# Kernel tuning notes

Measured on AMD Instinct MI355X. Metric: run time of the kernel, lower is better.

The kernel has to match this reference:

```python
import jax, jax.numpy as jnp
import numpy as np

N, E, F, D, H, L = 10000, 160000, 64, 32, 128, 2
DEG_HIST = np.zeros(17, np.float32); DEG_HIST[16] = N  # all nodes degree 16
BINS = np.arange(17, dtype=np.float32)
AVG_DEG_LOG = float((np.log(BINS + 1.0) * DEG_HIST).sum() / DEG_HIST.sum())
EPS_BN = 1e-5
EPS_STD = 1e-5


def setup_inputs() -> dict:
    key = jax.random.key(0)
    ks = iter(jax.random.split(key, 16))
    def w(shape, s=0.05):
        return jax.random.normal(next(ks), shape, dtype=jnp.float32) * s
    return {
        'x': jax.random.normal(next(ks), (N, F), dtype=jnp.float32),
        'edge_index': jax.random.randint(next(ks), (2, E), 0, N, dtype=jnp.int32),
        'edge_attr': jax.random.normal(next(ks), (E, D), dtype=jnp.float32),
        'W_node': w((F, H)), 'b_node': jnp.zeros((H,), jnp.float32),
        'W_edge': w((D, H)), 'b_edge': jnp.zeros((H,), jnp.float32),
        'W_ee': w((L, H, H)), 'b_ee': jnp.zeros((L, H), jnp.float32),
        'W_pre': w((L, 3 * H, H)), 'b_pre': jnp.zeros((L, H), jnp.float32),
        'W_post': w((L, 13 * H, H)), 'b_post': jnp.zeros((L, H), jnp.float32),
        'W_lin': w((L, H, H)), 'b_lin': jnp.zeros((L, H), jnp.float32),
        'gamma': jnp.ones((L, H), jnp.float32), 'beta': jnp.zeros((L, H), jnp.float32),
        'We1': w((L, 3 * H, H)), 'be1': jnp.zeros((L, H), jnp.float32),
        'We2': w((L, H, H)), 'be2': jnp.zeros((L, H), jnp.float32),
    }


def _pna_layer(x, edge_attr, src, dst, p):
    (W_ee, b_ee, W_pre, b_pre, W_post, b_post, W_lin, b_lin,
     gamma, beta, We1, be1, We2, be2) = p
    # message: pre-MLP on [x_i (dst), x_j (src), encoded edge_attr]
    e_enc = edge_attr @ W_ee + b_ee                                   # [E,H]
    h = jnp.concatenate([x[dst], x[src], e_enc], axis=-1) @ W_pre + b_pre  # [E,H]
    # multi-aggregator scatter at dst
    cnt = jax.ops.segment_sum(jnp.ones((E,), h.dtype), dst, num_segments=N)  # [N]
    degc = jnp.maximum(cnt, 1.0)[:, None]
    mean = jax.ops.segment_sum(h, dst, num_segments=N) / degc
    msq = jax.ops.segment_sum(h * h, dst, num_segments=N) / degc
    std = jnp.sqrt(jax.nn.relu(msq - mean * mean) + EPS_STD)
    has = (cnt > 0)[:, None]
    mn = jnp.where(has, jax.ops.segment_min(h, dst, num_segments=N), 0.0)
    mx = jnp.where(has, jax.ops.segment_max(h, dst, num_segments=N), 0.0)
    agg = jnp.concatenate([mean, mn, mx, std], axis=-1)               # [N,4H]
    # degree scalers: identity, amplification, attenuation
    f = jnp.log(degc + 1.0) / AVG_DEG_LOG
    scaled = jnp.concatenate([agg, agg * f, agg / f], axis=-1)        # [N,12H]
    out = jnp.concatenate([x, scaled], axis=-1) @ W_post + b_post     # [N,H]
    out = out @ W_lin + b_lin
    # BatchNorm (training mode: batch stats, biased var)
    mu = out.mean(axis=0)
    var = out.var(axis=0)
    bn = gamma * (out - mu) * jax.lax.rsqrt(var + EPS_BN) + beta
    x = (x + jax.nn.relu(bn)) / 2.0
    # edge update MLP
    eu = jnp.concatenate([x[src], x[dst], edge_attr], axis=-1)
    edge_attr = edge_attr + (jax.nn.relu(eu @ We1 + be1) @ We2 + be2) / 2.0
    return x, edge_attr


def reference(x, edge_index, edge_attr, W_node, b_node, W_edge, b_edge,
              W_ee, b_ee, W_pre, b_pre, W_post, b_post, W_lin, b_lin,
              gamma, beta, We1, be1, We2, be2):
    src, dst = edge_index[0], edge_index[1]
    xh = x @ W_node + b_node
    e = edge_attr @ W_edge + b_edge
    for i in range(L):
        p = (W_ee[i], b_ee[i], W_pre[i], b_pre[i], W_post[i], b_post[i],
             W_lin[i], b_lin[i], gamma[i], beta[i], We1[i], be1[i], We2[i], be2[i])
        xh, e = _pna_layer(xh, e, src, dst, p)
    return xh, e
```

## Files before the change

kernel.cpp:

```cpp
#include <hip/hip_runtime.h>

#define NODES 10000
#define EDGES 160000
#define FDIM 64
#define DDIM 32
#define HDIM 128
#define AVG_DEG_LOG 2.8332133440562162f
#define EPS_BN 1e-5f
#define EPS_STD 1e-5f

typedef short bf16x8 __attribute__((ext_vector_type(8)));
typedef float f32x4  __attribute__((ext_vector_type(4)));

struct GArgs {
  const float* A;
  const float* s0;
  const float* s1;
  const int*   i0;
  const int*   i1;
  const float* agg;
  const float* fs;
  const float* invfs;
  const float* B;
  const unsigned short* Bph;
  const unsigned short* Bpl;
  const float* bias;
  float*       C;
  int M, K;
};

__device__ __forceinline__ unsigned short f2bf(float x){
  unsigned u = __float_as_uint(x);
  return (unsigned short)((u + 0x7FFFu + ((u >> 16) & 1u)) >> 16);
}
__device__ __forceinline__ float bf2f(unsigned short h){
  return __uint_as_float(((unsigned)h) << 16);
}

#define BK 32
#define APAD 8
#define ASTR (BK + APAD)

template<int AMODE>
__device__ __forceinline__ void stage_load(const GArgs& g, int row0, int k0, float4 (&v)[4]){
  const int tid = threadIdx.x;
  const int r  = tid >> 1;
  const int c0 = (tid & 1) << 4;
  const int gr = row0 + r;
  if (gr >= g.M){
    v[0] = v[1] = v[2] = v[3] = make_float4(0.f, 0.f, 0.f, 0.f);
    return;
  }
  const int kk = k0 + c0;
  const float* p;
  float scale = 1.f;
  if constexpr (AMODE == 0){
    p = g.A + (size_t)gr * g.K + kk;
  } else if constexpr (AMODE == 1){
    if (kk < HDIM)          p = g.s0 + (size_t)g.i0[gr] * HDIM + kk;
    else if (kk < 2*HDIM)   p = g.s1 + (size_t)g.i1[gr] * HDIM + (kk - HDIM);
    else                    p = g.A  + (size_t)gr * HDIM + (kk - 2*HDIM);
  } else {
    if (kk < HDIM){
      p = g.A + (size_t)gr * HDIM + kk;
    } else {
      int q = kk - HDIM; int seg = q >> 9;
      p = g.agg + (size_t)gr * 512 + (q & 511);
      if (seg == 1)      scale = g.fs[gr];
      else if (seg == 2) scale = g.invfs[gr];
    }
  }
  const float4* p4 = (const float4*)p;
  v[0] = p4[0]; v[1] = p4[1]; v[2] = p4[2]; v[3] = p4[3];
  if (scale != 1.f){
    #pragma unroll
    for (int j = 0; j < 4; j++){
      v[j].x *= scale; v[j].y *= scale; v[j].z *= scale; v[j].w *= scale;
    }
  }
}

__device__ __forceinline__ void stage_write(unsigned short* __restrict__ AhB,
                                            unsigned short* __restrict__ AlB,
                                            const float4 (&v)[4]){
  const int tid = threadIdx.x;
  const int base = (tid >> 1) * ASTR + ((tid & 1) << 4);
  #pragma unroll
  for (int j = 0; j < 4; j++){
    ushort4 h, l;
    h.x = f2bf(v[j].x); l.x = f2bf(v[j].x - bf2f(h.x));
    h.y = f2bf(v[j].y); l.y = f2bf(v[j].y - bf2f(h.y));
    h.z = f2bf(v[j].z); l.z = f2bf(v[j].z - bf2f(h.z));
    h.w = f2bf(v[j].w); l.w = f2bf(v[j].w - bf2f(h.w));
    *(ushort4*)&AhB[base + j*4] = h;
    *(ushort4*)&AlB[base + j*4] = l;
  }
}

template<int AMODE, int EPI>
__global__ __launch_bounds__(256) void mgemm_k(GArgs g){
  __shared__ unsigned short Ah[2][128 * ASTR];
  __shared__ unsigned short Al[2][128 * ASTR];
  const int tid  = threadIdx.x;
  const int row0 = blockIdx.y * 128;
  const int wave = tid >> 6, lane = tid & 63;
  const int rh = wave >> 1, ch = wave & 1;
  const int lrow = lane & 15, lk = lane >> 4;

  f32x4 acc[4][4] = {};

  const int nsteps = g.K >> 5;
  float4 v[4];
  stage_load<AMODE>(g, row0, 0, v);
  stage_write(Ah[0], Al[0], v);
  __syncthreads();

  for (int s = 0; s < nsteps; s++){
    const int cur = s & 1, nxt = cur ^ 1;
    const bool have = (s + 1) < nsteps;
    if (have) stage_load<AMODE>(g, row0, (s + 1) << 5, v);

    bf16x8 bh[4], bl[4];
    const size_t bbase = ((size_t)s * 8 + ch * 4) * 64 * 8 + (size_t)lane * 8;
    #pragma unroll
    for (int nf = 0; nf < 4; nf++){
      bh[nf] = *(const bf16x8*)(g.Bph + bbase + (size_t)nf * 64 * 8);
      bl[nf] = *(const bf16x8*)(g.Bpl + bbase + (size_t)nf * 64 * 8);
    }
    #pragma unroll
    for (int mf = 0; mf < 4; mf++){
      const int ao = (rh*64 + mf*16 + lrow) * ASTR + lk * 8;
      bf16x8 ah  = *(const bf16x8*)&Ah[cur][ao];
      bf16x8 alo = *(const bf16x8*)&Al[cur][ao];
      #pragma unroll
      for (int nf = 0; nf < 4; nf++){
        acc[mf][nf] = __builtin_amdgcn_mfma_f32_16x16x32_bf16(ah,  bh[nf], acc[mf][nf], 0, 0, 0);
        acc[mf][nf] = __builtin_amdgcn_mfma_f32_16x16x32_bf16(ah,  bl[nf], acc[mf][nf], 0, 0, 0);
        acc[mf][nf] = __builtin_amdgcn_mfma_f32_16x16x32_bf16(alo, bh[nf], acc[mf][nf], 0, 0, 0);
      }
    }
    if (have) stage_write(Ah[nxt], Al[nxt], v);
    __syncthreads();
  }

  #pragma unroll
  for (int mf = 0; mf < 4; mf++){
    #pragma unroll
    for (int nf = 0; nf < 4; nf++){
      const int col = ch*64 + nf*16 + lrow;
      const float b = g.bias[col];
      #pragma unroll
      for (int j = 0; j < 4; j++){
        const int r = row0 + rh*64 + mf*16 + lk*4 + j;
        if (r < g.M){
          float val = acc[mf][nf][j] + b;
          if constexpr (EPI == 1) val = fmaxf(val, 0.f);
          float* cp = g.C + (size_t)r * HDIM + col;
          if constexpr (EPI == 2) val = *cp + 0.5f * val;
          *cp = val;
        }
      }
    }
  }
}

__global__ void bprep_k(const float* __restrict__ W, unsigned short* __restrict__ Bph,
                        unsigned short* __restrict__ Bpl){
  const int bb = blockIdx.x;
  const int kq = bb >> 3, n = bb & 7;
  const int l = threadIdx.x;
  const int colg = n*16 + (l & 15);
  const int krow = kq*32 + (l >> 4)*8;
  float vv[8];
  #pragma unroll
  for (int i = 0; i < 8; i++) vv[i] = W[(size_t)(krow + i) * HDIM + colg];
  ushort4 h0, h1, l0, l1;
  h0.x=f2bf(vv[0]); l0.x=f2bf(vv[0]-bf2f(h0.x));
  h0.y=f2bf(vv[1]); l0.y=f2bf(vv[1]-bf2f(h0.y));
  h0.z=f2bf(vv[2]); l0.z=f2bf(vv[2]-bf2f(h0.z));
  h0.w=f2bf(vv[3]); l0.w=f2bf(vv[3]-bf2f(h0.w));
  h1.x=f2bf(vv[4]); l1.x=f2bf(vv[4]-bf2f(h1.x));
  h1.y=f2bf(vv[5]); l1.y=f2bf(vv[5]-bf2f(h1.y));
  h1.z=f2bf(vv[6]); l1.z=f2bf(vv[6]-bf2f(h1.z));
  h1.w=f2bf(vv[7]); l1.w=f2bf(vv[7]-bf2f(h1.w));
  const size_t o = ((size_t)bb * 64 + l) * 8;
  *(ushort4*)&Bph[o]   = h0; *(ushort4*)&Bph[o+4] = h1;
  *(ushort4*)&Bpl[o]   = l0; *(ushort4*)&Bpl[o+4] = l1;
}

template<int AMODE_UNUSED, int EPI_UNUSED>
__global__ __launch_bounds__(256) void gemm_k(GArgs g){
  __shared__ float As[16][68];
  __shared__ float Bs[16][68];
  const int tid = threadIdx.x;
  const int tx = tid & 15, ty = tid >> 4;
  const int row0 = blockIdx.y * 64, col0 = blockIdx.x * 64;
  float acc[4][4] = {};
  for (int k0 = 0; k0 < g.K; k0 += 16){
    #pragma unroll
    for (int i = 0; i < 4; i++){
      int l = tid + i * 256;
      int ar = l >> 4, ak = l & 15;
      int gr = row0 + ar;
      float v = 0.f;
      if (gr < g.M) v = g.A[(size_t)gr * g.K + k0 + ak];
      As[ak][ar] = v;
    }
    #pragma unroll
    for (int i = 0; i < 4; i++){
      int l = tid + i * 256;
      int bn_ = l & 63, bk = l >> 6;
      Bs[bk][bn_] = g.B[(size_t)(k0 + bk) * HDIM + col0 + bn_];
    }
    __syncthreads();
    #pragma unroll
    for (int kk = 0; kk < 16; kk++){
      float a[4], b[4];
      #pragma unroll
      for (int j = 0; j < 4; j++) a[j] = As[kk][ty*4 + j];
      #pragma unroll
      for (int j = 0; j < 4; j++) b[j] = Bs[kk][tx*4 + j];
      #pragma unroll
      for (int ii = 0; ii < 4; ii++)
        #pragma unroll
        for (int jj = 0; jj < 4; jj++)
          acc[ii][jj] = fmaf(a[ii], b[jj], acc[ii][jj]);
    }
    __syncthreads();
  }
  #pragma unroll
  for (int ii = 0; ii < 4; ii++){
    int gr = row0 + ty*4 + ii;
    if (gr >= g.M) continue;
    #pragma unroll
    for (int jj = 0; jj < 4; jj++)
      g.C[(size_t)gr * HDIM + col0 + tx*4 + jj] = acc[ii][jj];
  }
}

__global__ void deg_init_k(int* cnt, int* cursor){
  int i = blockIdx.x * 256 + threadIdx.x;
  if (i < NODES){ cnt[i] = 0; cursor[i] = 0; }
}
__global__ void deg_count_k(const int* __restrict__ dst, int* cnt){
  int e = blockIdx.x * 256 + threadIdx.x;
  if (e < EDGES) atomicAdd(&cnt[dst[e]], 1);
}
__global__ void deg_fin_k(const int* __restrict__ cnt, float* fdeg, float* invf){
  int i = blockIdx.x * 256 + threadIdx.x;
  if (i < NODES){
    float d = fmaxf((float)cnt[i], 1.f);
    float f = logf(d + 1.f) / AVG_DEG_LOG;
    fdeg[i] = f;
    invf[i] = 1.f / f;
  }
}
__global__ __launch_bounds__(256) void scan_k(const int* __restrict__ cnt, int* __restrict__ off){
  __shared__ int sh[256];
  __shared__ int carry;
  if (threadIdx.x == 0) carry = 0;
  __syncthreads();
  for (int base = 0; base < NODES; base += 256){
    int i = base + threadIdx.x;
    int v = (i < NODES) ? cnt[i] : 0;
    sh[threadIdx.x] = v;
    __syncthreads();
    #pragma unroll
    for (int o = 1; o < 256; o <<= 1){
      int t = (threadIdx.x >= o) ? sh[threadIdx.x - o] : 0;
      __syncthreads();
      sh[threadIdx.x] += t;
      __syncthreads();
    }
    if (i < NODES) off[i] = carry + sh[threadIdx.x] - v;
    __syncthreads();
    if (threadIdx.x == 255) carry += sh[255];
    __syncthreads();
  }
  if (threadIdx.x == 0) off[NODES] = carry;
}
__global__ void csr_fill_k(const int* __restrict__ dst, const int* __restrict__ off,
                           int* cursor, int* __restrict__ eidx){
  int e = blockIdx.x * 256 + threadIdx.x;
  if (e < EDGES){
    int d = dst[e];
    int p = atomicAdd(&cursor[d], 1);
    eidx[off[d] + p] = e;
  }
}

__global__ __launch_bounds__(256) void aggregate_k(const float* __restrict__ h,
                                                   const int* __restrict__ off,
                                                   const int* __restrict__ eidx,
                                                   float* __restrict__ agg){
  const int node = blockIdx.x * 2 + (threadIdx.x >> 7);
  const int c = threadIdx.x & 127;
  if (node >= NODES) return;
  const int o0 = off[node], o1 = off[node + 1];
  const int d  = o1 - o0;
  float s = 0.f, ss = 0.f, mn = INFINITY, mx = -INFINITY;
  for (int k = o0; k < o1; k++){
    float vv = h[(size_t)eidx[k] * HDIM + c];
    s += vv; ss += vv * vv;
    mn = fminf(mn, vv); mx = fmaxf(mx, vv);
  }
  const float degc = fmaxf((float)d, 1.f);
  const float mean = s / degc;
  const float msq  = ss / degc;
  const float sd   = sqrtf(fmaxf(msq - mean * mean, 0.f) + EPS_STD);
  if (d == 0){ mn = 0.f; mx = 0.f; }
  float* a = agg + (size_t)node * 512;
  a[c]       = mean;
  a[128 + c] = mn;
  a[256 + c] = mx;
  a[384 + c] = sd;
}

__global__ __launch_bounds__(256) void bn_stats_k(const float* __restrict__ out2, float* mu, float* var){
  __shared__ float sh1[256], sh2[256];
  int c = blockIdx.x;
  float s = 0.f, ss = 0.f;
  for (int r = threadIdx.x; r < NODES; r += 256){
    float v = out2[(size_t)r * HDIM + c];
    s += v; ss += v * v;
  }
  sh1[threadIdx.x] = s; sh2[threadIdx.x] = ss;
  __syncthreads();
  for (int o = 128; o > 0; o >>= 1){
    if (threadIdx.x < o){ sh1[threadIdx.x] += sh1[threadIdx.x + o]; sh2[threadIdx.x] += sh2[threadIdx.x + o]; }
    __syncthreads();
  }
  if (threadIdx.x == 0){
    float m = sh1[0] / (float)NODES;
    mu[c] = m;
    var[c] = sh2[0] / (float)NODES - m * m;
  }
}

__global__ void xh_update_k(float* __restrict__ xh, const float* __restrict__ out2,
                            const float* __restrict__ mu, const float* __restrict__ var,
                            const float* __restrict__ gamma, const float* __restrict__ beta){
  int i = blockIdx.x * 256 + threadIdx.x;
  if (i >= NODES * HDIM) return;
  int c = i & 127;
  float bn = gamma[c] * (out2[i] - mu[c]) * rsqrtf(var[c] + EPS_BN) + beta[c];
  xh[i] = (xh[i] + fmaxf(bn, 0.f)) * 0.5f;
}

__global__ void copy_k(float* __restrict__ d, const float* __restrict__ s, int n){
  int i = blockIdx.x * 256 + threadIdx.x;
  if (i < n) d[i] = s[i];
}
__global__ void bias_comb_k(const float* __restrict__ bin, const float* __restrict__ W,
                            const float* __restrict__ badd, float* __restrict__ bout){
  int j = threadIdx.x;
  float s = badd[j];
  for (int k = 0; k < HDIM; k++) s = fmaf(bin[k], W[(size_t)k * HDIM + j], s);
  bout[j] = s;
}

extern "C" void kernel_launch(void* const* d_in, const int* in_sizes, int n_in,
                              void* d_out, int out_size, void* d_ws, size_t ws_size,
                              hipStream_t stream) {
  const float* x      = (const float*)d_in[0];
  const int*   ei     = (const int*)  d_in[1];
  const float* ea     = (const float*)d_in[2];
  const float* W_node = (const float*)d_in[3];
  const float* b_node = (const float*)d_in[4];
  const float* W_edge = (const float*)d_in[5];
  const float* b_edge = (const float*)d_in[6];
  const float* W_ee   = (const float*)d_in[7];
  const float* b_ee   = (const float*)d_in[8];
  const float* W_pre  = (const float*)d_in[9];
  const float* b_pre  = (const float*)d_in[10];
  const float* W_post = (const float*)d_in[11];
  const float* b_post = (const float*)d_in[12];
  const float* W_lin  = (const float*)d_in[13];
  const float* b_lin  = (const float*)d_in[14];
  const float* gamma  = (const float*)d_in[15];
  const float* beta   = (const float*)d_in[16];
  const float* We1    = (const float*)d_in[17];
  const float* be1    = (const float*)d_in[18];
  const float* We2    = (const float*)d_in[19];
  const float* be2    = (const float*)d_in[20];

  const int* src = ei;
  const int* dst = ei + EDGES;

  float* xh = (float*)d_out;
  float* e  = xh + (size_t)NODES * HDIM;

  char* wp = (char*)d_ws;
  auto alloc = [&](size_t bytes) -> char* {
    char* r = wp;
    wp += (bytes + 63) & ~(size_t)63;
    return r;
  };
  float* h     = (float*)alloc((size_t)EDGES * HDIM * 4);
  float* agg   = (float*)alloc((size_t)NODES * 512 * 4);
  float* out2  = (float*)alloc((size_t)NODES * HDIM * 4);
  int*   cnt    = (int*)alloc(NODES * 4);
  int*   cursor = (int*)alloc(NODES * 4);
  int*   off    = (int*)alloc((NODES + 1) * 4);
  int*   eidx   = (int*)alloc(EDGES * 4);
  float* fdeg = (float*)alloc(NODES * 4);
  float* invf = (float*)alloc(NODES * 4);
  float* Wc1  = (float*)alloc(384 * HDIM * 4);
  float* Wc2  = (float*)alloc(1664 * HDIM * 4);
  float* bc1  = (float*)alloc(HDIM * 4);
  float* bc2  = (float*)alloc(HDIM * 4);
  float* mu   = (float*)alloc(HDIM * 4);
  float* var  = (float*)alloc(HDIM * 4);
  auto allocS = [&](int K) -> unsigned short* { return (unsigned short*)alloc((size_t)K * HDIM * 2); };
  unsigned short* BpNh = allocS(64);   unsigned short* BpNl = allocS(64);
  unsigned short* BpEh = allocS(32);   unsigned short* BpEl = allocS(32);
  unsigned short* Bp1h = allocS(384);  unsigned short* Bp1l = allocS(384);
  unsigned short* Bp2h = allocS(1664); unsigned short* Bp2l = allocS(1664);
  unsigned short* Bp3h = allocS(384);  unsigned short* Bp3l = allocS(384);
  unsigned short* Bp4h = allocS(128);  unsigned short* Bp4l = allocS(128);

  dim3 blk(256);
  auto mgrid = [](int M){ return dim3(1, (M + 127) / 128); };
  auto bgrid = [](int K){ return dim3((K / 32) * 8); };

  GArgs g{};

  deg_init_k <<<(NODES + 255) / 256, blk, 0, stream>>>(cnt, cursor);
  deg_count_k<<<(EDGES + 255) / 256, blk, 0, stream>>>(dst, cnt);
  deg_fin_k  <<<(NODES + 255) / 256, blk, 0, stream>>>(cnt, fdeg, invf);
  scan_k     <<<1, blk, 0, stream>>>(cnt, off);
  csr_fill_k <<<(EDGES + 255) / 256, blk, 0, stream>>>(dst, off, cursor, eidx);

  bprep_k<<<bgrid(FDIM), 64, 0, stream>>>(W_node, BpNh, BpNl);
  bprep_k<<<bgrid(DDIM), 64, 0, stream>>>(W_edge, BpEh, BpEl);

  g = GArgs{}; g.A = x; g.Bph = BpNh; g.Bpl = BpNl; g.bias = b_node; g.C = xh;
  g.M = NODES; g.K = FDIM;
  mgemm_k<0,0><<<mgrid(NODES), blk, 0, stream>>>(g);

  g = GArgs{}; g.A = ea; g.Bph = BpEh; g.Bpl = BpEl; g.bias = b_edge; g.C = e;
  g.M = EDGES; g.K = DDIM;
  mgemm_k<0,0><<<mgrid(EDGES), blk, 0, stream>>>(g);

  for (int l = 0; l < 2; l++){
    const float* W_ee_l   = W_ee   + (size_t)l * HDIM * HDIM;
    const float* b_ee_l   = b_ee   + l * HDIM;
    const float* W_pre_l  = W_pre  + (size_t)l * 3 * HDIM * HDIM;
    const float* b_pre_l  = b_pre  + l * HDIM;
    const float* W_post_l = W_post + (size_t)l * 13 * HDIM * HDIM;
    const float* b_post_l = b_post + l * HDIM;
    const float* W_lin_l  = W_lin  + (size_t)l * HDIM * HDIM;
    const float* b_lin_l  = b_lin  + l * HDIM;
    const float* gamma_l  = gamma  + l * HDIM;
    const float* beta_l   = beta   + l * HDIM;
    const float* We1_l    = We1    + (size_t)l * 3 * HDIM * HDIM;
    const float* be1_l    = be1    + l * HDIM;
    const float* We2_l    = We2    + (size_t)l * HDIM * HDIM;
    const float* be2_l    = be2    + l * HDIM;
    const float* Wp3      = W_pre_l + (size_t)2 * HDIM * HDIM;

    copy_k<<<(2 * HDIM * HDIM + 255) / 256, blk, 0, stream>>>(Wc1, W_pre_l, 2 * HDIM * HDIM);
    g = GArgs{}; g.A = W_ee_l; g.B = Wp3; g.C = Wc1 + (size_t)2 * HDIM * HDIM;
    g.M = HDIM; g.K = HDIM;
    gemm_k<0,0><<<dim3(2, 2), blk, 0, stream>>>(g);
    bias_comb_k<<<1, HDIM, 0, stream>>>(b_ee_l, Wp3, b_pre_l, bc1);
    bprep_k<<<bgrid(3 * HDIM), 64, 0, stream>>>(Wc1, Bp1h, Bp1l);

    g = GArgs{}; g.A = e; g.s0 = xh; g.s1 = xh; g.i0 = dst; g.i1 = src;
    g.Bph = Bp1h; g.Bpl = Bp1l; g.bias = bc1; g.C = h; g.M = EDGES; g.K = 3 * HDIM;
    mgemm_k<1,0><<<mgrid(EDGES), blk, 0, stream>>>(g);

    aggregate_k<<<(NODES + 1) / 2, blk, 0, stream>>>(h, off, eidx, agg);

    g = GArgs{}; g.A = W_post_l; g.B = W_lin_l; g.C = Wc2; g.M = 13 * HDIM; g.K = HDIM;
    gemm_k<0,0><<<dim3(2, 26), blk, 0, stream>>>(g);
    bias_comb_k<<<1, HDIM, 0, stream>>>(b_post_l, W_lin_l, b_lin_l, bc2);
    bprep_k<<<bgrid(13 * HDIM), 64, 0, stream>>>(Wc2, Bp2h, Bp2l);

    g = GArgs{}; g.A = xh; g.agg = agg; g.fs = fdeg; g.invfs = invf;
    g.Bph = Bp2h; g.Bpl = Bp2l; g.bias = bc2; g.C = out2; g.M = NODES; g.K = 13 * HDIM;
    mgemm_k<2,0><<<mgrid(NODES), blk, 0, stream>>>(g);

    bn_stats_k<<<HDIM, blk, 0, stream>>>(out2, mu, var);
    xh_update_k<<<(NODES * HDIM + 255) / 256, blk, 0, stream>>>(xh, out2, mu, var, gamma_l, beta_l);

    bprep_k<<<bgrid(3 * HDIM), 64, 0, stream>>>(We1_l, Bp3h, Bp3l);
    g = GArgs{}; g.A = e; g.s0 = xh; g.s1 = xh; g.i0 = src; g.i1 = dst;
    g.Bph = Bp3h; g.Bpl = Bp3l; g.bias = be1_l; g.C = h; g.M = EDGES; g.K = 3 * HDIM;
    mgemm_k<1,1><<<mgrid(EDGES), blk, 0, stream>>>(g);

    bprep_k<<<bgrid(HDIM), 64, 0, stream>>>(We2_l, Bp4h, Bp4l);
    g = GArgs{}; g.A = h; g.Bph = Bp4h; g.Bpl = Bp4l; g.bias = be2_l; g.C = e;
    g.M = EDGES; g.K = HDIM;
    mgemm_k<0,2><<<mgrid(EDGES), blk, 0, stream>>>(g);
  }
}
```

Baseline: 1.027 ms.

## Use 512-thread MFMA GEMM blocks with hoisted row pointers and deeper prefetch

```diff
diff --git a/kernel.cpp b/kernel.cpp
--- a/kernel.cpp
+++ b/kernel.cpp
@@ -10,6 +10,7 @@
 #define EPS_STD 1e-5f
 
 typedef short bf16x8 __attribute__((ext_vector_type(8)));
+typedef unsigned short u16x8 __attribute__((ext_vector_type(8)));
 typedef float f32x4  __attribute__((ext_vector_type(4)));
 
 struct GArgs {
@@ -37,99 +38,105 @@
   return __uint_as_float(((unsigned)h) << 16);
 }
 
-#define BK 32
-#define APAD 8
-#define ASTR (BK + APAD)
-
-template<int AMODE>
-__device__ __forceinline__ void stage_load(const GArgs& g, int row0, int k0, float4 (&v)[4]){
-  const int tid = threadIdx.x;
-  const int r  = tid >> 1;
-  const int c0 = (tid & 1) << 4;
-  const int gr = row0 + r;
-  if (gr >= g.M){
-    v[0] = v[1] = v[2] = v[3] = make_float4(0.f, 0.f, 0.f, 0.f);
-    return;
-  }
-  const int kk = k0 + c0;
-  const float* p;
-  float scale = 1.f;
-  if constexpr (AMODE == 0){
-    p = g.A + (size_t)gr * g.K + kk;
-  } else if constexpr (AMODE == 1){
-    if (kk < HDIM)          p = g.s0 + (size_t)g.i0[gr] * HDIM + kk;
-    else if (kk < 2*HDIM)   p = g.s1 + (size_t)g.i1[gr] * HDIM + (kk - HDIM);
-    else                    p = g.A  + (size_t)gr * HDIM + (kk - 2*HDIM);
-  } else {
-    if (kk < HDIM){
-      p = g.A + (size_t)gr * HDIM + kk;
-    } else {
-      int q = kk - HDIM; int seg = q >> 9;
-      p = g.agg + (size_t)gr * 512 + (q & 511);
-      if (seg == 1)      scale = g.fs[gr];
-      else if (seg == 2) scale = g.invfs[gr];
-    }
-  }
-  const float4* p4 = (const float4*)p;
-  v[0] = p4[0]; v[1] = p4[1]; v[2] = p4[2]; v[3] = p4[3];
-  if (scale != 1.f){
-    #pragma unroll
-    for (int j = 0; j < 4; j++){
-      v[j].x *= scale; v[j].y *= scale; v[j].z *= scale; v[j].w *= scale;
-    }
-  }
-}
-
-__device__ __forceinline__ void stage_write(unsigned short* __restrict__ AhB,
-                                            unsigned short* __restrict__ AlB,
-                                            const float4 (&v)[4]){
-  const int tid = threadIdx.x;
-  const int base = (tid >> 1) * ASTR + ((tid & 1) << 4);
-  #pragma unroll
-  for (int j = 0; j < 4; j++){
-    ushort4 h, l;
-    h.x = f2bf(v[j].x); l.x = f2bf(v[j].x - bf2f(h.x));
-    h.y = f2bf(v[j].y); l.y = f2bf(v[j].y - bf2f(h.y));
-    h.z = f2bf(v[j].z); l.z = f2bf(v[j].z - bf2f(h.z));
-    h.w = f2bf(v[j].w); l.w = f2bf(v[j].w - bf2f(h.w));
-    *(ushort4*)&AhB[base + j*4] = h;
-    *(ushort4*)&AlB[base + j*4] = l;
-  }
-}
+#define ASTR 40
 
 template<int AMODE, int EPI>
-__global__ __launch_bounds__(256) void mgemm_k(GArgs g){
+__global__ __launch_bounds__(512, 4) void mgemm_k(GArgs g){
   __shared__ unsigned short Ah[2][128 * ASTR];
   __shared__ unsigned short Al[2][128 * ASTR];
   const int tid  = threadIdx.x;
   const int row0 = blockIdx.y * 128;
   const int wave = tid >> 6, lane = tid & 63;
-  const int rh = wave >> 1, ch = wave & 1;
+  const int rq = wave >> 1, ch = wave & 1;
   const int lrow = lane & 15, lk = lane >> 4;
 
-  f32x4 acc[4][4] = {};
+  const int srow = tid >> 2;
+  const int c0   = (tid & 3) << 3;
+  const int gr   = row0 + srow;
+  const bool valid = gr < g.M;
+  const int gi = valid ? gr : 0;
+  const float* p0; const float* p1; const float* p2;
+  float f1 = 1.f, f2 = 1.f;
+  if constexpr (AMODE == 0){
+    p0 = g.A + (size_t)gi * g.K; p1 = p0; p2 = p0;
+  } else if constexpr (AMODE == 1){
+    p0 = g.s0 + (size_t)g.i0[gi] * HDIM;
+    p1 = g.s1 + (size_t)g.i1[gi] * HDIM;
+    p2 = g.A  + (size_t)gi * HDIM;
+  } else {
+    p0 = g.A   + (size_t)gi * HDIM;
+    p1 = g.agg + (size_t)gi * 512;
+    p2 = p1;
+    f1 = g.fs[gi]; f2 = g.invfs[gi];
+  }
+
+  auto ld8 = [&](int k0, float4& a, float4& b){
+    if (!valid){ a = make_float4(0.f,0.f,0.f,0.f); b = a; return; }
+    const int kk = k0 + c0;
+    const float* p; float sc = 1.f;
+    if constexpr (AMODE == 0){
+      p = p0 + kk;
+    } else if constexpr (AMODE == 1){
+      p = (kk < HDIM) ? (p0 + kk) : (kk < 2*HDIM) ? (p1 + kk - HDIM) : (p2 + kk - 2*HDIM);
+    } else {
+      if (kk < HDIM){ p = p0 + kk; }
+      else {
+        const int q = kk - HDIM;
+        p = p1 + (q & 511);
+        const int seg = q >> 9;
+        sc = (seg == 0) ? 1.f : (seg == 1) ? f1 : f2;
+      }
+    }
+    const float4* p4 = (const float4*)p;
+    a = p4[0]; b = p4[1];
+    if constexpr (AMODE == 2){
+      if (sc != 1.f){
+        a.x*=sc; a.y*=sc; a.z*=sc; a.w*=sc;
+        b.x*=sc; b.y*=sc; b.z*=sc; b.w*=sc;
+      }
+    }
+  };
+
+  auto st8 = [&](int buf, const float4& a, const float4& b){
+    const int base = srow * ASTR + c0;
+    const float vv[8] = {a.x,a.y,a.z,a.w,b.x,b.y,b.z,b.w};
+    u16x8 h8, l8;
+    #pragma unroll
+    for (int j = 0; j < 8; j++){
+      const unsigned u = __float_as_uint(vv[j]);
+      h8[j] = (unsigned short)(u >> 16);
+      const float rem = vv[j] - __uint_as_float(u & 0xFFFF0000u);
+      l8[j] = (unsigned short)(__float_as_uint(rem) >> 16);
+    }
+    *(u16x8*)&Ah[buf][base] = h8;
+    *(u16x8*)&Al[buf][base] = l8;
+  };
 
   const int nsteps = g.K >> 5;
-  float4 v[4];
-  stage_load<AMODE>(g, row0, 0, v);
-  stage_write(Ah[0], Al[0], v);
+  float4 va, vb, wa, wb;
+  ld8(0, va, vb);
+  st8(0, va, vb);
+  if (nsteps > 1) ld8(32, wa, wb);
   __syncthreads();
 
+  f32x4 acc[2][4] = {};
+
   for (int s = 0; s < nsteps; s++){
-    const int cur = s & 1, nxt = cur ^ 1;
-    const bool have = (s + 1) < nsteps;
-    if (have) stage_load<AMODE>(g, row0, (s + 1) << 5, v);
-
+    const int cur = s & 1;
     bf16x8 bh[4], bl[4];
-    const size_t bbase = ((size_t)s * 8 + ch * 4) * 64 * 8 + (size_t)lane * 8;
+    const size_t bbase = ((size_t)s * 8 + ch * 4) * 512 + (size_t)lane * 8;
     #pragma unroll
     for (int nf = 0; nf < 4; nf++){
-      bh[nf] = *(const bf16x8*)(g.Bph + bbase + (size_t)nf * 64 * 8);
-      bl[nf] = *(const bf16x8*)(g.Bpl + bbase + (size_t)nf * 64 * 8);
-    }
-    #pragma unroll
-    for (int mf = 0; mf < 4; mf++){
-      const int ao = (rh*64 + mf*16 + lrow) * ASTR + lk * 8;
+      bh[nf] = *(const bf16x8*)(g.Bph + bbase + (size_t)nf * 512);
+      bl[nf] = *(const bf16x8*)(g.Bpl + bbase + (size_t)nf * 512);
+    }
+    if (s + 1 < nsteps){
+      st8(cur ^ 1, wa, wb);
+      if (s + 2 < nsteps) ld8((s + 2) << 5, wa, wb);
+    }
+    #pragma unroll
+    for (int mf = 0; mf < 2; mf++){
+      const int ao = (rq*32 + mf*16 + lrow) * ASTR + lk * 8;
       bf16x8 ah  = *(const bf16x8*)&Ah[cur][ao];
       bf16x8 alo = *(const bf16x8*)&Al[cur][ao];
       #pragma unroll
@@ -139,19 +146,18 @@
         acc[mf][nf] = __builtin_amdgcn_mfma_f32_16x16x32_bf16(alo, bh[nf], acc[mf][nf], 0, 0, 0);
       }
     }
-    if (have) stage_write(Ah[nxt], Al[nxt], v);
     __syncthreads();
   }
 
   #pragma unroll
-  for (int mf = 0; mf < 4; mf++){
+  for (int mf = 0; mf < 2; mf++){
     #pragma unroll
     for (int nf = 0; nf < 4; nf++){
       const int col = ch*64 + nf*16 + lrow;
       const float b = g.bias[col];
       #pragma unroll
       for (int j = 0; j < 4; j++){
-        const int r = row0 + rh*64 + mf*16 + lk*4 + j;
+        const int r = row0 + rq*32 + mf*16 + lk*4 + j;
         if (r < g.M){
           float val = acc[mf][nf][j] + b;
           if constexpr (EPI == 1) val = fmaxf(val, 0.f);
@@ -174,18 +180,15 @@
   float vv[8];
   #pragma unroll
   for (int i = 0; i < 8; i++) vv[i] = W[(size_t)(krow + i) * HDIM + colg];
-  ushort4 h0, h1, l0, l1;
-  h0.x=f2bf(vv[0]); l0.x=f2bf(vv[0]-bf2f(h0.x));
-  h0.y=f2bf(vv[1]); l0.y=f2bf(vv[1]-bf2f(h0.y));
-  h0.z=f2bf(vv[2]); l0.z=f2bf(vv[2]-bf2f(h0.z));
-  h0.w=f2bf(vv[3]); l0.w=f2bf(vv[3]-bf2f(h0.w));
-  h1.x=f2bf(vv[4]); l1.x=f2bf(vv[4]-bf2f(h1.x));
-  h1.y=f2bf(vv[5]); l1.y=f2bf(vv[5]-bf2f(h1.y));
-  h1.z=f2bf(vv[6]); l1.z=f2bf(vv[6]-bf2f(h1.z));
-  h1.w=f2bf(vv[7]); l1.w=f2bf(vv[7]-bf2f(h1.w));
+  u16x8 h, lo;
+  #pragma unroll
+  for (int i = 0; i < 8; i++){
+    h[i]  = f2bf(vv[i]);
+    lo[i] = f2bf(vv[i] - bf2f(h[i]));
+  }
   const size_t o = ((size_t)bb * 64 + l) * 8;
-  *(ushort4*)&Bph[o]   = h0; *(ushort4*)&Bph[o+4] = h1;
-  *(ushort4*)&Bpl[o]   = l0; *(ushort4*)&Bpl[o+4] = l1;
+  *(u16x8*)&Bph[o] = h;
+  *(u16x8*)&Bpl[o] = lo;
 }
 
 template<int AMODE_UNUSED, int EPI_UNUSED>
@@ -420,6 +423,7 @@
   unsigned short* Bp4h = allocS(128);  unsigned short* Bp4l = allocS(128);
 
   dim3 blk(256);
+  dim3 blk512(512);
   auto mgrid = [](int M){ return dim3(1, (M + 127) / 128); };
   auto bgrid = [](int K){ return dim3((K / 32) * 8); };
 
@@ -436,11 +440,11 @@
 
   g = GArgs{}; g.A = x; g.Bph = BpNh; g.Bpl = BpNl; g.bias = b_node; g.C = xh;
   g.M = NODES; g.K = FDIM;
-  mgemm_k<0,0><<<mgrid(NODES), blk, 0, stream>>>(g);
+  mgemm_k<0,0><<<mgrid(NODES), blk512, 0, stream>>>(g);
 
   g = GArgs{}; g.A = ea; g.Bph = BpEh; g.Bpl = BpEl; g.bias = b_edge; g.C = e;
   g.M = EDGES; g.K = DDIM;
-  mgemm_k<0,0><<<mgrid(EDGES), blk, 0, stream>>>(g);
+  mgemm_k<0,0><<<mgrid(EDGES), blk512, 0, stream>>>(g);
 
   for (int l = 0; l < 2; l++){
     const float* W_ee_l   = W_ee   + (size_t)l * HDIM * HDIM;
@@ -468,7 +472,7 @@
 
     g = GArgs{}; g.A = e; g.s0 = xh; g.s1 = xh; g.i0 = dst; g.i1 = src;
     g.Bph = Bp1h; g.Bpl = Bp1l; g.bias = bc1; g.C = h; g.M = EDGES; g.K = 3 * HDIM;
-    mgemm_k<1,0><<<mgrid(EDGES), blk, 0, stream>>>(g);
+    mgemm_k<1,0><<<mgrid(EDGES), blk512, 0, stream>>>(g);
 
     aggregate_k<<<(NODES + 1) / 2, blk, 0, stream>>>(h, off, eidx, agg);
 
@@ -479,7 +483,7 @@
 
     g = GArgs{}; g.A = xh; g.agg = agg; g.fs = fdeg; g.invfs = invf;
     g.Bph = Bp2h; g.Bpl = Bp2l; g.bias = bc2; g.C = out2; g.M = NODES; g.K = 13 * HDIM;
-    mgemm_k<2,0><<<mgrid(NODES), blk, 0, stream>>>(g);
+    mgemm_k<2,0><<<mgrid(NODES), blk512, 0, stream>>>(g);
 
     bn_stats_k<<<HDIM, blk, 0, stream>>>(out2, mu, var);
     xh_update_k<<<(NODES * HDIM + 255) / 256, blk, 0, stream>>>(xh, out2, mu, var, gamma_l, beta_l);
@@ -487,11 +491,11 @@
     bprep_k<<<bgrid(3 * HDIM), 64, 0, stream>>>(We1_l, Bp3h, Bp3l);
     g = GArgs{}; g.A = e; g.s0 = xh; g.s1 = xh; g.i0 = src; g.i1 = dst;
     g.Bph = Bp3h; g.Bpl = Bp3l; g.bias = be1_l; g.C = h; g.M = EDGES; g.K = 3 * HDIM;
-    mgemm_k<1,1><<<mgrid(EDGES), blk, 0, stream>>>(g);
+    mgemm_k<1,1><<<mgrid(EDGES), blk512, 0, stream>>>(g);
 
     bprep_k<<<bgrid(HDIM), 64, 0, stream>>>(We2_l, Bp4h, Bp4l);
     g = GArgs{}; g.A = h; g.Bph = Bp4h; g.Bpl = Bp4l; g.bias = be2_l; g.C = e;
     g.M = EDGES; g.K = HDIM;
-    mgemm_k<0,2><<<mgrid(EDGES), blk, 0, stream>>>(g);
-  }
-}
+    mgemm_k<0,2><<<mgrid(EDGES), blk512, 0, stream>>>(g);
+  }
+}
```

Result: slower. 1.122 ms (+9.3%).
